# Performance work log

Hardware: AMD Instinct MI355X
Metric: run time of the kernel (lower is better)

Reference implementation:

```python
import jax, jax.numpy as jnp
import numpy as np

B, ENC, DEC, H, W = 8, 64, 128, 128, 128
NEG = -1e30  # masked-softmax fill


def _neighbors(x):
    """x: [B,H,W,C] -> [B,H,W,9,C] 3x3 neighborhood gather (zeros at borders)."""
    b, h, w, c = x.shape
    p = jnp.pad(x, ((0, 0), (1, 1), (1, 1), (0, 0)))
    return jnp.stack([p[:, r:r + h, c_:c_ + w, :] for r in range(3) for c_ in range(3)], axis=3)


def _neighbor_mask(h, w):
    """[H,W,9] bool: which of the 9 neighbors are in-bounds per pixel."""
    m = jnp.pad(jnp.ones((h, w), dtype=bool), ((1, 1), (1, 1)))
    return jnp.stack([m[r:r + h, c_:c_ + w] for r in range(3) for c_ in range(3)], axis=2)


def setup_inputs() -> dict:
    key = jax.random.key(0)
    ks = jax.random.split(key, 12)
    s = 0.05
    return {
        "encoder_features": jax.random.normal(ks[0], (B, ENC, H, W), jnp.float32),
        "decoder_features": jax.random.normal(ks[1], (B, DEC, H, W), jnp.float32),
        "W_enc": jax.random.normal(ks[2], (ENC, ENC), jnp.float32) * s,
        "b_enc": jax.random.normal(ks[3], (ENC,), jnp.float32) * s,
        "W_dec": jax.random.normal(ks[4], (DEC, ENC), jnp.float32) * s,
        "b_dec": jax.random.normal(ks[5], (ENC,), jnp.float32) * s,
        "W_agg": jax.random.normal(ks[6], (ENC, 1), jnp.float32) * s,
        "b_agg": jax.random.normal(ks[7], (1,), jnp.float32) * s,
        "W_attn": jax.random.normal(ks[8], (2 * ENC, ENC), jnp.float32) * s,
        "b_attn": jax.random.normal(ks[9], (ENC,), jnp.float32) * s,
        "conv_w": jax.random.normal(ks[10], (3, 3, DEC, ENC), jnp.float32) * s,  # HWIO
        "conv_b": jax.random.normal(ks[11], (ENC,), jnp.float32) * s,
    }


def reference(encoder_features, decoder_features, W_enc, b_enc, W_dec, b_dec,
              W_agg, b_agg, W_attn, b_attn, conv_w, conv_b):
    # NCHW -> NHWC (format_linear)
    enc = jnp.transpose(encoder_features, (0, 2, 3, 1))  # [B,H,W,ENC]
    dec = jnp.transpose(decoder_features, (0, 2, 3, 1))  # [B,H,W,DEC]

    q = dec @ W_dec + b_dec  # [B,H,W,ENC]
    k = enc @ W_enc + b_enc  # [B,H,W,ENC]
    vals = jax.lax.conv_general_dilated(
        dec, conv_w, window_strides=(1, 1), padding='SAME',
        dimension_numbers=('NHWC', 'HWIO', 'NHWC')) + conv_b  # [B,H,W,ENC]

    kn = _neighbors(k)    # [B,H,W,9,ENC]
    en = _neighbors(enc)  # [B,H,W,9,ENC]
    mask = _neighbor_mask(q.shape[1], q.shape[2])  # [H,W,9]

    # per-neighbor additive score: agg_encoder(tanh(query + key)) -> scalar
    scores = jnp.squeeze(jnp.tanh(q[:, :, :, None, :] + kn) @ W_agg, -1) + b_agg  # [B,H,W,9]
    scores = jnp.where(mask, scores, NEG)
    attn_w = jax.nn.softmax(scores, axis=-1)  # softmax over valid neighbors only
    attn_vec = jnp.einsum('bhwn,bhwnc->bhwc', attn_w, en)  # weighted sum of raw encoder feats

    cat = jnp.concatenate([vals, attn_vec], axis=-1)  # [B,H,W,2*ENC]
    out = cat @ W_attn + b_attn
    out = jnp.where(out >= 0, out, 0.2 * out)  # LeakyReLU(0.2)
    return jnp.transpose(out, (0, 3, 1, 2))  # back to NCHW
```

## Files before the change

### kernel.cpp

```cpp
#include <hip/hip_runtime.h>

#define BB 8
#define ENC_C 64
#define DEC_C 128
#define HH 128
#define WW 128

typedef unsigned short ushort_t;
typedef __attribute__((ext_vector_type(8))) short short8;
typedef __attribute__((ext_vector_type(4))) float f32x4;

static __device__ __forceinline__ ushort_t f2bf(float x) {
  unsigned int u = __builtin_bit_cast(unsigned int, x);
  u += 0x7fff + ((u >> 16) & 1);
  return (ushort_t)(u >> 16);
}
static __device__ __forceinline__ float bf2f(ushort_t v) {
  unsigned int u = ((unsigned int)v) << 16;
  return __builtin_bit_cast(float, u);
}

__global__ __launch_bounds__(64) void pack_w_kernel(
    const float* __restrict__ conv_w, const float* __restrict__ W_attn,
    const float* __restrict__ W_dec, const float* __restrict__ W_enc,
    ushort_t* __restrict__ packedC, ushort_t* __restrict__ packedA,
    ushort_t* __restrict__ packedQ, ushort_t* __restrict__ packedK)
{
  const int blk = blockIdx.x;
  const int l = threadIdx.x;
  const float* W;
  ushort_t* dst;
  int bb;
  if (blk < 144) {
    const int kstep = blk >> 2, nf = blk & 3;
    const int tap = kstep >> 2, dstep = kstep & 3;
    const int n = nf * 16 + (l & 15);
    const int dbase = dstep * 32 + (l >> 4) * 8;
    ushort_t v[8];
    #pragma unroll
    for (int j = 0; j < 8; ++j)
      v[j] = f2bf(conv_w[(tap * DEC_C + dbase + j) * 64 + n]);
    ushort_t* d = packedC + ((long)blk * 64 + l) * 8;
    #pragma unroll
    for (int j = 0; j < 8; ++j) d[j] = v[j];
    return;
  } else if (blk < 160) {
    W = W_attn; dst = packedA; bb = blk - 144;
  } else if (blk < 176) {
    W = W_dec;  dst = packedQ; bb = blk - 160;
  } else {
    W = W_enc;  dst = packedK; bb = blk - 176;
  }
  const int ks = bb >> 2, nf = bb & 3;
  const int n = nf * 16 + (l & 15);
  const int kbase = ks * 32 + (l >> 4) * 8;
  ushort_t v[8];
  #pragma unroll
  for (int j = 0; j < 8; ++j)
    v[j] = f2bf(W[(kbase + j) * 64 + n]);
  ushort_t* d = dst + ((long)bb * 64 + l) * 8;
  #pragma unroll
  for (int j = 0; j < 8; ++j) d[j] = v[j];
}

__global__ __launch_bounds__(256) void prep_kernel(
    const float* __restrict__ enc, const float* __restrict__ dec,
    const ushort_t* __restrict__ packedQ, const ushort_t* __restrict__ packedK,
    const float* __restrict__ b_enc, const float* __restrict__ b_dec,
    ushort_t* __restrict__ q_nhwc, ushort_t* __restrict__ k_nhwc,
    ushort_t* __restrict__ enc_t, ushort_t* __restrict__ dec_t)
{
  __shared__ float smem[WW * 68];
  const int bh = blockIdx.x;
  const int b = bh >> 7, h = bh & 127;
  const int tid = threadIdx.x;
  const int l = tid & 63;
  const int wv = tid >> 6;
  const int pix0 = wv * 32;
  const int col = l & 15, kg = l >> 4;

  #pragma unroll
  for (int i = 0; i < 32; ++i) {
    int idx = tid + i * 256;
    int cc = idx >> 7, wl = idx & 127;
    smem[wl * 68 + cc] = enc[((b * ENC_C + cc) * HH + h) * WW + wl];
  }
  __syncthreads();

  #pragma unroll
  for (int i = 0; i < 32; ++i) {
    int idx = tid + i * 256;
    int wl = idx >> 6, cc = idx & 63;
    enc_t[((long)bh * WW + wl) * 64 + cc] = f2bf(smem[wl * 68 + cc]);
  }

  f32x4 acck[2][4];
  #pragma unroll
  for (int mf = 0; mf < 2; ++mf)
    #pragma unroll
    for (int nf = 0; nf < 4; ++nf)
      acck[mf][nf] = (f32x4){0.f, 0.f, 0.f, 0.f};

  #pragma unroll
  for (int ks = 0; ks < 2; ++ks) {
    short8 afr[2];
    #pragma unroll
    for (int mf = 0; mf < 2; ++mf) {
      const int pix = pix0 + mf * 16 + col;
      const float4* p = (const float4*)&smem[pix * 68 + ks * 32 + kg * 8];
      float4 x0 = p[0], x1 = p[1];
      short8 v;
      v[0] = (short)f2bf(x0.x); v[1] = (short)f2bf(x0.y);
      v[2] = (short)f2bf(x0.z); v[3] = (short)f2bf(x0.w);
      v[4] = (short)f2bf(x1.x); v[5] = (short)f2bf(x1.y);
      v[6] = (short)f2bf(x1.z); v[7] = (short)f2bf(x1.w);
      afr[mf] = v;
    }
    #pragma unroll
    for (int nf = 0; nf < 4; ++nf) {
      const short8 bfr =
          *(const short8*)(packedK + ((long)(ks * 4 + nf) * 64 + l) * 8);
      acck[0][nf] = __builtin_amdgcn_mfma_f32_16x16x32_bf16(
          afr[0], bfr, acck[0][nf], 0, 0, 0);
      acck[1][nf] = __builtin_amdgcn_mfma_f32_16x16x32_bf16(
          afr[1], bfr, acck[1][nf], 0, 0, 0);
    }
  }
  #pragma unroll
  for (int mf = 0; mf < 2; ++mf)
    #pragma unroll
    for (int nf = 0; nf < 4; ++nf)
      #pragma unroll
      for (int r = 0; r < 4; ++r) {
        const int pix = pix0 + mf * 16 + kg * 4 + r;
        const int c = nf * 16 + col;
        k_nhwc[((long)bh * WW + pix) * 64 + c] = f2bf(acck[mf][nf][r] + b_enc[c]);
      }
  __syncthreads();

  f32x4 accq[2][4];
  #pragma unroll
  for (int mf = 0; mf < 2; ++mf)
    #pragma unroll
    for (int nf = 0; nf < 4; ++nf)
      accq[mf][nf] = (f32x4){0.f, 0.f, 0.f, 0.f};

  #pragma unroll
  for (int hf = 0; hf < 2; ++hf) {
    #pragma unroll
    for (int i = 0; i < 32; ++i) {
      int idx = tid + i * 256;
      int cc = idx >> 7, wl = idx & 127;
      smem[wl * 68 + cc] = dec[((b * DEC_C + hf * 64 + cc) * HH + h) * WW + wl];
    }
    __syncthreads();

    #pragma unroll
    for (int i = 0; i < 32; ++i) {
      int idx = tid + i * 256;
      int wl = idx >> 6, cc = idx & 63;
      dec_t[((long)bh * WW + wl) * DEC_C + hf * 64 + cc] =
          f2bf(smem[wl * 68 + cc]);
    }

    #pragma unroll
    for (int ks2 = 0; ks2 < 2; ++ks2) {
      const int ks = hf * 2 + ks2;
      short8 afr[2];
      #pragma unroll
      for (int mf = 0; mf < 2; ++mf) {
        const int pix = pix0 + mf * 16 + col;
        const float4* p = (const float4*)&smem[pix * 68 + ks2 * 32 + kg * 8];
        float4 x0 = p[0], x1 = p[1];
        short8 v;
        v[0] = (short)f2bf(x0.x); v[1] = (short)f2bf(x0.y);
        v[2] = (short)f2bf(x0.z); v[3] = (short)f2bf(x0.w);
        v[4] = (short)f2bf(x1.x); v[5] = (short)f2bf(x1.y);
        v[6] = (short)f2bf(x1.z); v[7] = (short)f2bf(x1.w);
        afr[mf] = v;
      }
      #pragma unroll
      for (int nf = 0; nf < 4; ++nf) {
        const short8 bfr =
            *(const short8*)(packedQ + ((long)(ks * 4 + nf) * 64 + l) * 8);
        accq[0][nf] = __builtin_amdgcn_mfma_f32_16x16x32_bf16(
            afr[0], bfr, accq[0][nf], 0, 0, 0);
        accq[1][nf] = __builtin_amdgcn_mfma_f32_16x16x32_bf16(
            afr[1], bfr, accq[1][nf], 0, 0, 0);
      }
    }
    __syncthreads();
  }

  #pragma unroll
  for (int mf = 0; mf < 2; ++mf)
    #pragma unroll
    for (int nf = 0; nf < 4; ++nf)
      #pragma unroll
      for (int r = 0; r < 4; ++r) {
        const int pix = pix0 + mf * 16 + kg * 4 + r;
        const int c = nf * 16 + col;
        q_nhwc[((long)bh * WW + pix) * 64 + c] = f2bf(accq[mf][nf][r] + b_dec[c]);
      }
}

__global__ __launch_bounds__(256) void attn_kernel(
    const ushort_t* __restrict__ q_nhwc, const ushort_t* __restrict__ k_nhwc,
    const ushort_t* __restrict__ enc_t, const float* __restrict__ W_agg,
    const float* __restrict__ b_agg, ushort_t* __restrict__ att)
{
  const int nwg = gridDim.x;
  const int cpx = nwg >> 3;
  const int bid = blockIdx.x;
  const int swz = (bid & 7) * cpx + (bid >> 3);
  const int t = swz * 256 + threadIdx.x;
  const int h = (t >> 7) & 127;
  const int w = t & 127;

  int off[9]; bool valid[9];
  #pragma unroll
  for (int n = 0; n < 9; ++n) {
    const int dh = n / 3 - 1, dw = n % 3 - 1;
    const int nh = h + dh, nw = w + dw;
    valid[n] = (nh >= 0 && nh < HH && nw >= 0 && nw < WW);
    const int nhc = min(max(nh, 0), HH - 1);
    const int nwc = min(max(nw, 0), WW - 1);
    off[n] = (t & ~16383) + nhc * WW + nwc;
  }

  const short8* qp = (const short8*)(q_nhwc + ((long)t << 6));
  const short8* kp[9];
  const short8* ep[9];
  #pragma unroll
  for (int n = 0; n < 9; ++n) {
    kp[n] = (const short8*)(k_nhwc + ((long)off[n] << 6));
    ep[n] = (const short8*)(enc_t + ((long)off[n] << 6));
  }

  float s[9];
  #pragma unroll
  for (int n = 0; n < 9; ++n) s[n] = 0.f;

  for (int ci = 0; ci < 4; ++ci) {
    const short8 qa = qp[2 * ci], qb = qp[2 * ci + 1];
    float wa[16];
    #pragma unroll
    for (int e = 0; e < 16; ++e) wa[e] = W_agg[ci * 16 + e];
    #pragma unroll
    for (int n = 0; n < 9; ++n) {
      const short8 ka = kp[n][2 * ci], kb = kp[n][2 * ci + 1];
      float sc = 0.f;
      #pragma unroll
      for (int e = 0; e < 8; ++e) {
        float x = bf2f((ushort_t)qa[e]) + bf2f((ushort_t)ka[e]);
        x = fminf(fmaxf(x, -15.f), 15.f);
        float z = __builtin_amdgcn_exp2f(x * 2.88539008f);
        float tt = __builtin_fmaf(-2.f, __builtin_amdgcn_rcpf(z + 1.f), 1.f);
        sc = __builtin_fmaf(tt, wa[e], sc);
      }
      #pragma unroll
      for (int e = 0; e < 8; ++e) {
        float x = bf2f((ushort_t)qb[e]) + bf2f((ushort_t)kb[e]);
        x = fminf(fmaxf(x, -15.f), 15.f);
        float z = __builtin_amdgcn_exp2f(x * 2.88539008f);
        float tt = __builtin_fmaf(-2.f, __builtin_amdgcn_rcpf(z + 1.f), 1.f);
        sc = __builtin_fmaf(tt, wa[8 + e], sc);
      }
      s[n] += sc;
    }
  }

  const float bagg = b_agg[0];
  float m = -1e30f;
  #pragma unroll
  for (int n = 0; n < 9; ++n) {
    s[n] = valid[n] ? (s[n] + bagg) : -1e30f;
    m = fmaxf(m, s[n]);
  }
  float attw[9]; float denom = 0.f;
  #pragma unroll
  for (int n = 0; n < 9; ++n) {
    attw[n] = __builtin_amdgcn_exp2f((s[n] - m) * 1.44269504f);
    denom += attw[n];
  }
  const float inv = __builtin_amdgcn_rcpf(denom);
  #pragma unroll
  for (int n = 0; n < 9; ++n) attw[n] *= inv;

  short8* op = (short8*)(att + ((long)t << 6));
  for (int ci = 0; ci < 4; ++ci) {
    float a16[16];
    #pragma unroll
    for (int e = 0; e < 16; ++e) a16[e] = 0.f;
    #pragma unroll
    for (int n = 0; n < 9; ++n) {
      const short8 ea = ep[n][2 * ci], eb = ep[n][2 * ci + 1];
      #pragma unroll
      for (int e = 0; e < 8; ++e)
        a16[e] = __builtin_fmaf(attw[n], bf2f((ushort_t)ea[e]), a16[e]);
      #pragma unroll
      for (int e = 0; e < 8; ++e)
        a16[8 + e] = __builtin_fmaf(attw[n], bf2f((ushort_t)eb[e]), a16[8 + e]);
    }
    short8 o0, o1;
    #pragma unroll
    for (int e = 0; e < 8; ++e) {
      o0[e] = (short)f2bf(a16[e]);
      o1[e] = (short)f2bf(a16[8 + e]);
    }
    op[2 * ci] = o0;
    op[2 * ci + 1] = o1;
  }
}

__global__ __launch_bounds__(256, 3) void conv_out_kernel(
    const ushort_t* __restrict__ dec_t, const ushort_t* __restrict__ packedC,
    const float* __restrict__ conv_b, const ushort_t* __restrict__ attn_nhwc,
    const ushort_t* __restrict__ packedA, const float* __restrict__ b_attn,
    float* __restrict__ out)
{
  __shared__ ushort_t bsh[24576];
  ushort_t* vlds = bsh;
  const int nwg = gridDim.x;
  const int cpx = nwg >> 3;
  const int bid = blockIdx.x;
  const int bh = (bid & 7) * cpx + (bid >> 3);
  const int b = bh >> 7, h = bh & 127;
  const int tid = threadIdx.x;
  const int l = tid & 63;
  const int wv = tid >> 6;
  const int pix0 = wv * 32;
  const int col = l & 15, kg = l >> 4;

  f32x4 acc[2][4];
  #pragma unroll
  for (int mf = 0; mf < 2; ++mf)
    #pragma unroll
    for (int nf = 0; nf < 4; ++nf)
      acc[mf][nf] = (f32x4){0.f, 0.f, 0.f, 0.f};

  #pragma unroll
  for (int kh = 0; kh < 3; ++kh) {
    const int hh = h + kh - 1;
    if (hh < 0 || hh >= HH) continue;
    __syncthreads();
    {
      const short8* src = (const short8*)(packedC + (long)kh * 24576);
      #pragma unroll
      for (int i = 0; i < 12; ++i)
        *(short8*)&bsh[(tid + i * 256) * 8] = src[tid + i * 256];
    }
    __syncthreads();

    const ushort_t* arow = dec_t + ((long)(b * HH + hh) * WW) * DEC_C;
    #pragma unroll
    for (int ds = 0; ds < 4; ++ds) {
      const int d0 = ds * 32;
      short8 afr[3][2];
      #pragma unroll
      for (int kw = 0; kw < 3; ++kw)
        #pragma unroll
        for (int mf = 0; mf < 2; ++mf) {
          const int wp = pix0 + mf * 16 + col + kw - 1;
          short8 v = {0, 0, 0, 0, 0, 0, 0, 0};
          if (wp >= 0 && wp < WW)
            v = *(const short8*)(arow + (long)wp * DEC_C + d0 + kg * 8);
          afr[kw][mf] = v;
        }
      #pragma unroll
      for (int kw = 0; kw < 3; ++kw) {
        #pragma unroll
        for (int nf = 0; nf < 4; ++nf) {
          const short8 bfr =
              *(const short8*)&bsh[(((kw * 4 + ds) * 4 + nf) * 64 + l) * 8];
          acc[0][nf] = __builtin_amdgcn_mfma_f32_16x16x32_bf16(
              afr[kw][0], bfr, acc[0][nf], 0, 0, 0);
          acc[1][nf] = __builtin_amdgcn_mfma_f32_16x16x32_bf16(
              afr[kw][1], bfr, acc[1][nf], 0, 0, 0);
        }
      }
    }
  }

  __syncthreads();
  #pragma unroll
  for (int mf = 0; mf < 2; ++mf)
    #pragma unroll
    for (int nf = 0; nf < 4; ++nf)
      #pragma unroll
      for (int r = 0; r < 4; ++r) {
        const int pix = pix0 + mf * 16 + kg * 4 + r;
        const int c = nf * 16 + col;
        vlds[pix * 72 + c] = f2bf(acc[mf][nf][r] + conv_b[c]);
      }
  __syncthreads();

  f32x4 ao[4][2];
  #pragma unroll
  for (int mf = 0; mf < 4; ++mf)
    #pragma unroll
    for (int pf = 0; pf < 2; ++pf)
      ao[mf][pf] = (f32x4){0.f, 0.f, 0.f, 0.f};

  #pragma unroll
  for (int ks = 0; ks < 4; ++ks) {
    short8 bfr[2];
    #pragma unroll
    for (int pf = 0; pf < 2; ++pf) {
      const int pix = pix0 + pf * 16 + col;
      short8 v;
      if (ks < 2) {
        v = *(const short8*)&vlds[pix * 72 + ks * 32 + kg * 8];
      } else {
        v = *(const short8*)(attn_nhwc + ((long)bh * WW + pix) * 64 +
                             (ks - 2) * 32 + kg * 8);
      }
      bfr[pf] = v;
    }
    #pragma unroll
    for (int mf = 0; mf < 4; ++mf) {
      const short8 afr =
          *(const short8*)(packedA + ((long)(ks * 4 + mf) * 64 + l) * 8);
      #pragma unroll
      for (int pf = 0; pf < 2; ++pf)
        ao[mf][pf] = __builtin_amdgcn_mfma_f32_16x16x32_bf16(
            afr, bfr[pf], ao[mf][pf], 0, 0, 0);
    }
  }

  #pragma unroll
  for (int mf = 0; mf < 4; ++mf)
    #pragma unroll
    for (int pf = 0; pf < 2; ++pf)
      #pragma unroll
      for (int r = 0; r < 4; ++r) {
        const int n = mf * 16 + kg * 4 + r;
        const int pix = pix0 + pf * 16 + col;
        float o = ao[mf][pf][r] + b_attn[n];
        o = (o >= 0.f) ? o : 0.2f * o;
        out[((long)(b * ENC_C + n) * HH + h) * WW + pix] = o;
      }
}

extern "C" void kernel_launch(void* const* d_in, const int* in_sizes, int n_in,
                              void* d_out, int out_size, void* d_ws, size_t ws_size,
                              hipStream_t stream) {
  const float* enc    = (const float*)d_in[0];
  const float* dec    = (const float*)d_in[1];
  const float* W_enc  = (const float*)d_in[2];
  const float* b_enc  = (const float*)d_in[3];
  const float* W_dec  = (const float*)d_in[4];
  const float* b_dec  = (const float*)d_in[5];
  const float* W_agg  = (const float*)d_in[6];
  const float* b_agg  = (const float*)d_in[7];
  const float* W_attn = (const float*)d_in[8];
  const float* b_attn = (const float*)d_in[9];
  const float* conv_w = (const float*)d_in[10];
  const float* conv_b = (const float*)d_in[11];
  float* out = (float*)d_out;

  const long npix = (long)BB * HH * WW;
  ushort_t* q_bf    = (ushort_t*)d_ws;
  ushort_t* k_bf    = q_bf + npix * 64;
  ushort_t* enc_t   = k_bf + npix * 64;
  ushort_t* dec_t   = enc_t + npix * 64;
  ushort_t* att     = dec_t + npix * 128;
  ushort_t* packedC = att + npix * 64;
  ushort_t* packedA = packedC + 144 * 64 * 8;
  ushort_t* packedQ = packedA + 16 * 64 * 8;
  ushort_t* packedK = packedQ + 16 * 64 * 8;

  hipLaunchKernelGGL(pack_w_kernel, dim3(184), dim3(64), 0, stream,
                     conv_w, W_attn, W_dec, W_enc, packedC, packedA, packedQ, packedK);
  hipLaunchKernelGGL(prep_kernel, dim3(BB * HH), dim3(256), 0, stream,
                     enc, dec, packedQ, packedK, b_enc, b_dec, q_bf, k_bf, enc_t, dec_t);
  hipLaunchKernelGGL(attn_kernel, dim3((int)(npix / 256)), dim3(256), 0, stream,
                     q_bf, k_bf, enc_t, W_agg, b_agg, att);
  hipLaunchKernelGGL(conv_out_kernel, dim3(BB * HH), dim3(256), 0, stream,
                     dec_t, packedC, conv_b, att, packedA, b_attn, out);
}
```

Measured before the change: 146.9 us.

## Process two output rows per workgroup in conv_out to reuse staged weights

The fused conv and output-projection kernel now has each 256-thread workgroup compute two adjacent image rows instead of one, and the grid is halved. Each LDS-staged block of 3x3 conv weights is then used for twice as many MFMAs, which halves weight staging traffic and barriers per output row. In exchange, each thread holds twice as many accumulators and A fragments, which raises register pressure. The min-occupancy launch bound is dropped, border rows now run zero-filled MFMAs instead of being skipped, and only 512 workgroups are launched, which may leave some compute units underused.

```diff
diff --git a/kernel.cpp b/kernel.cpp
--- a/kernel.cpp
+++ b/kernel.cpp
@@ -313,7 +313,7 @@
   }
 }
 
-__global__ __launch_bounds__(256, 3) void conv_out_kernel(
+__global__ __launch_bounds__(256) void conv_out_kernel(
     const ushort_t* __restrict__ dec_t, const ushort_t* __restrict__ packedC,
     const float* __restrict__ conv_b, const ushort_t* __restrict__ attn_nhwc,
     const ushort_t* __restrict__ packedA, const float* __restrict__ b_attn,
@@ -324,25 +324,26 @@
   const int nwg = gridDim.x;
   const int cpx = nwg >> 3;
   const int bid = blockIdx.x;
-  const int bh = (bid & 7) * cpx + (bid >> 3);
-  const int b = bh >> 7, h = bh & 127;
+  const int grp = (bid & 7) * cpx + (bid >> 3);
+  const int b = grp >> 6;
+  const int h0 = (grp & 63) * 2;
   const int tid = threadIdx.x;
   const int l = tid & 63;
   const int wv = tid >> 6;
   const int pix0 = wv * 32;
   const int col = l & 15, kg = l >> 4;
 
-  f32x4 acc[2][4];
-  #pragma unroll
-  for (int mf = 0; mf < 2; ++mf)
-    #pragma unroll
-    for (int nf = 0; nf < 4; ++nf)
-      acc[mf][nf] = (f32x4){0.f, 0.f, 0.f, 0.f};
+  f32x4 acc[2][2][4];
+  #pragma unroll
+  for (int r = 0; r < 2; ++r)
+    #pragma unroll
+    for (int mf = 0; mf < 2; ++mf)
+      #pragma unroll
+      for (int nf = 0; nf < 4; ++nf)
+        acc[r][mf][nf] = (f32x4){0.f, 0.f, 0.f, 0.f};
 
   #pragma unroll
   for (int kh = 0; kh < 3; ++kh) {
-    const int hh = h + kh - 1;
-    if (hh < 0 || hh >= HH) continue;
     __syncthreads();
     {
       const short8* src = (const short8*)(packedC + (long)kh * 24576);
@@ -352,20 +353,27 @@
     }
     __syncthreads();
 
-    const ushort_t* arow = dec_t + ((long)(b * HH + hh) * WW) * DEC_C;
+    const int hh0 = h0 + kh - 1;
+    const bool v0 = (hh0 >= 0);
+    const bool v1 = (h0 + kh <= HH - 1);
+    const ushort_t* arow0 = dec_t + ((long)(b * HH + (v0 ? hh0 : 0)) * WW) * DEC_C;
+    const ushort_t* arow1 = dec_t + ((long)(b * HH + (v1 ? hh0 + 1 : 0)) * WW) * DEC_C;
+
     #pragma unroll
     for (int ds = 0; ds < 4; ++ds) {
       const int d0 = ds * 32;
-      short8 afr[3][2];
+      short8 afr[2][3][2];
       #pragma unroll
       for (int kw = 0; kw < 3; ++kw)
         #pragma unroll
         for (int mf = 0; mf < 2; ++mf) {
           const int wp = pix0 + mf * 16 + col + kw - 1;
-          short8 v = {0, 0, 0, 0, 0, 0, 0, 0};
-          if (wp >= 0 && wp < WW)
-            v = *(const short8*)(arow + (long)wp * DEC_C + d0 + kg * 8);
-          afr[kw][mf] = v;
+          const bool wok = (wp >= 0 && wp < WW);
+          short8 z = {0, 0, 0, 0, 0, 0, 0, 0};
+          afr[0][kw][mf] = (wok && v0)
+              ? *(const short8*)(arow0 + (long)wp * DEC_C + d0 + kg * 8) : z;
+          afr[1][kw][mf] = (wok && v1)
+              ? *(const short8*)(arow1 + (long)wp * DEC_C + d0 + kg * 8) : z;
         }
       #pragma unroll
       for (int kw = 0; kw < 3; ++kw) {
@@ -373,10 +381,13 @@
         for (int nf = 0; nf < 4; ++nf) {
           const short8 bfr =
               *(const short8*)&bsh[(((kw * 4 + ds) * 4 + nf) * 64 + l) * 8];
-          acc[0][nf] = __builtin_amdgcn_mfma_f32_16x16x32_bf16(
-              afr[kw][0], bfr, acc[0][nf], 0, 0, 0);
-          acc[1][nf] = __builtin_amdgcn_mfma_f32_16x16x32_bf16(
-              afr[kw][1], bfr, acc[1][nf], 0, 0, 0);
+          #pragma unroll
+          for (int r = 0; r < 2; ++r) {
+            acc[r][0][nf] = __builtin_amdgcn_mfma_f32_16x16x32_bf16(
+                afr[r][kw][0], bfr, acc[r][0][nf], 0, 0, 0);
+            acc[r][1][nf] = __builtin_amdgcn_mfma_f32_16x16x32_bf16(
+                afr[r][kw][1], bfr, acc[r][1][nf], 0, 0, 0);
+          }
         }
       }
     }
@@ -384,62 +395,67 @@
 
   __syncthreads();
   #pragma unroll
-  for (int mf = 0; mf < 2; ++mf)
-    #pragma unroll
-    for (int nf = 0; nf < 4; ++nf)
-      #pragma unroll
-      for (int r = 0; r < 4; ++r) {
-        const int pix = pix0 + mf * 16 + kg * 4 + r;
-        const int c = nf * 16 + col;
-        vlds[pix * 72 + c] = f2bf(acc[mf][nf][r] + conv_b[c]);
-      }
+  for (int r = 0; r < 2; ++r)
+    #pragma unroll
+    for (int mf = 0; mf < 2; ++mf)
+      #pragma unroll
+      for (int nf = 0; nf < 4; ++nf)
+        #pragma unroll
+        for (int rr = 0; rr < 4; ++rr) {
+          const int pix = pix0 + mf * 16 + kg * 4 + rr;
+          const int c = nf * 16 + col;
+          vlds[(r * WW + pix) * 72 + c] = f2bf(acc[r][mf][nf][rr] + conv_b[c]);
+        }
   __syncthreads();
 
-  f32x4 ao[4][2];
-  #pragma unroll
-  for (int mf = 0; mf < 4; ++mf)
-    #pragma unroll
-    for (int pf = 0; pf < 2; ++pf)
-      ao[mf][pf] = (f32x4){0.f, 0.f, 0.f, 0.f};
-
-  #pragma unroll
-  for (int ks = 0; ks < 4; ++ks) {
-    short8 bfr[2];
-    #pragma unroll
-    for (int pf = 0; pf < 2; ++pf) {
-      const int pix = pix0 + pf * 16 + col;
-      short8 v;
-      if (ks < 2) {
-        v = *(const short8*)&vlds[pix * 72 + ks * 32 + kg * 8];
-      } else {
-        v = *(const short8*)(attn_nhwc + ((long)bh * WW + pix) * 64 +
-                             (ks - 2) * 32 + kg * 8);
-      }
-      bfr[pf] = v;
-    }
-    #pragma unroll
-    for (int mf = 0; mf < 4; ++mf) {
-      const short8 afr =
-          *(const short8*)(packedA + ((long)(ks * 4 + mf) * 64 + l) * 8);
+  for (int r = 0; r < 2; ++r) {
+    const int bh = b * HH + h0 + r;
+    f32x4 ao[4][2];
+    #pragma unroll
+    for (int mf = 0; mf < 4; ++mf)
       #pragma unroll
       for (int pf = 0; pf < 2; ++pf)
-        ao[mf][pf] = __builtin_amdgcn_mfma_f32_16x16x32_bf16(
-            afr, bfr[pf], ao[mf][pf], 0, 0, 0);
-    }
-  }
-
-  #pragma unroll
-  for (int mf = 0; mf < 4; ++mf)
-    #pragma unroll
-    for (int pf = 0; pf < 2; ++pf)
-      #pragma unroll
-      for (int r = 0; r < 4; ++r) {
-        const int n = mf * 16 + kg * 4 + r;
+        ao[mf][pf] = (f32x4){0.f, 0.f, 0.f, 0.f};
+
+    #pragma unroll
+    for (int ks = 0; ks < 4; ++ks) {
+      short8 bfr[2];
+      #pragma unroll
+      for (int pf = 0; pf < 2; ++pf) {
         const int pix = pix0 + pf * 16 + col;
-        float o = ao[mf][pf][r] + b_attn[n];
-        o = (o >= 0.f) ? o : 0.2f * o;
-        out[((long)(b * ENC_C + n) * HH + h) * WW + pix] = o;
-      }
+        short8 v;
+        if (ks < 2) {
+          v = *(const short8*)&vlds[(r * WW + pix) * 72 + ks * 32 + kg * 8];
+        } else {
+          v = *(const short8*)(attn_nhwc + ((long)bh * WW + pix) * 64 +
+                               (ks - 2) * 32 + kg * 8);
+        }
+        bfr[pf] = v;
+      }
+      #pragma unroll
+      for (int mf = 0; mf < 4; ++mf) {
+        const short8 afr =
+            *(const short8*)(packedA + ((long)(ks * 4 + mf) * 64 + l) * 8);
+        #pragma unroll
+        for (int pf = 0; pf < 2; ++pf)
+          ao[mf][pf] = __builtin_amdgcn_mfma_f32_16x16x32_bf16(
+              afr, bfr[pf], ao[mf][pf], 0, 0, 0);
+      }
+    }
+
+    #pragma unroll
+    for (int mf = 0; mf < 4; ++mf)
+      #pragma unroll
+      for (int pf = 0; pf < 2; ++pf)
+        #pragma unroll
+        for (int rr = 0; rr < 4; ++rr) {
+          const int n = mf * 16 + kg * 4 + rr;
+          const int pix = pix0 + pf * 16 + col;
+          float o = ao[mf][pf][rr] + b_attn[n];
+          o = (o >= 0.f) ? o : 0.2f * o;
+          out[((long)(b * ENC_C + n) * HH + (h0 + r)) * WW + pix] = o;
+        }
+  }
 }
 
 extern "C" void kernel_launch(void* const* d_in, const int* in_sizes, int n_in,
@@ -476,6 +492,6 @@
                      enc, dec, packedQ, packedK, b_enc, b_dec, q_bf, k_bf, enc_t, dec_t);
   hipLaunchKernelGGL(attn_kernel, dim3((int)(npix / 256)), dim3(256), 0, stream,
                      q_bf, k_bf, enc_t, W_agg, b_agg, att);
-  hipLaunchKernelGGL(conv_out_kernel, dim3(BB * HH), dim3(256), 0, stream,
+  hipLaunchKernelGGL(conv_out_kernel, dim3(BB * HH / 2), dim3(256), 0, stream,
                      dec_t, packedC, conv_b, att, packedA, b_attn, out);
 }
```

Measured after the change: 145.7 us. Within noise of the previous version (-0.8%).
